# Performance work log

Measured on AMD Instinct MI355X. Metric: run time of the kernel, lower is better.

## Reference

```python
import jax, jax.numpy as jnp
import numpy as np

B, C, H, W = 32, 512, 32, 32
R = C // 2  # reduced channels for key/prod projections


def setup_inputs() -> dict:
    key = jax.random.key(0)
    ks = jax.random.split(key, 8)
    s_in = 1.0 / np.sqrt(C)
    return {
        "x": jax.random.normal(ks[0], (B, C, H, W), jnp.float32),
        "Wk": jax.random.normal(ks[1], (R, C), jnp.float32) * s_in,
        "bk": jax.random.normal(ks[2], (R,), jnp.float32) * s_in,
        "Wp": jax.random.normal(ks[3], (R, C), jnp.float32) * s_in,
        "bp": jax.random.normal(ks[4], (R,), jnp.float32) * s_in,
        "Wv": jax.random.normal(ks[5], (C, C), jnp.float32) * s_in,
        "bv": jax.random.normal(ks[6], (C,), jnp.float32) * s_in,
        "param": jax.random.normal(ks[7], (1,), jnp.float32),
    }


def _conv1x1(x, Wmat, b):
    # 1x1 conv on NCHW == per-pixel channel matmul
    return jnp.einsum('bchw,oc->bohw', x, Wmat) + b[None, :, None, None]


def reference(x, Wk, bk, Wp, bp, Wv, bv, param):
    b, c, h, w = x.shape
    hw = h * w
    f_key = _conv1x1(x, Wk, bk).reshape(b, -1, hw).transpose(0, 2, 1)  # [B,HW,R]
    f_prod = _conv1x1(x, Wp, bp).reshape(b, -1, hw)                    # [B,R,HW]
    f_value = _conv1x1(x, Wv, bv).reshape(b, -1, hw)                   # [B,C,HW]
    energy = jnp.einsum('bnr,brm->bnm', f_key, f_prod)                 # [B,HW,HW]
    similarity = jax.nn.softmax(energy, axis=-1)
    # bmm(f_value, similarity^T): out[b,c,n] = sum_m f_value[b,c,m] * sim[b,n,m]
    attended = jnp.einsum('bcm,bnm->bcn', f_value, similarity).reshape(b, c, h, w)
    return x + attended * param
```

## Files before the change

### kernel.cpp

```cpp
#include <hip/hip_runtime.h>
#include <hip/hip_bf16.h>

#define BATCH 32
#define CCH   512
#define HWSZ  1024
#define RCH   256

typedef __attribute__((ext_vector_type(8))) _Float16 f16x8;
typedef __attribute__((ext_vector_type(4))) float f32x4;

__device__ __forceinline__ ushort f2h(float f) {
    _Float16 h = (_Float16)f;
    ushort u; __builtin_memcpy(&u, &h, 2);
    return u;
}

__device__ __forceinline__ void load_lds16(const void* g, void* l) {
    __builtin_amdgcn_global_load_lds((const __attribute__((address_space(1))) void*)g,
                                     (__attribute__((address_space(3))) void*)l,
                                     16, 0, 0);
}

__device__ __forceinline__ void xcd_swizzle(int& bx, int& by, int& bz) {
    int gx = gridDim.x, gy = gridDim.y;
    int n   = gx * gy * gridDim.z;
    int lin = bx + gx * (by + gy * bz);
    int cpx = n >> 3;
    int s = (lin & 7) * cpx + (lin >> 3);
    bx = s % gx; s /= gx;
    by = s % gy;
    bz = s / gy;
}

__global__ __launch_bounds__(256) void k_prep_w(
    const float* __restrict__ Wk, const float* __restrict__ bk,
    const float* __restrict__ Wp, const float* __restrict__ bp,
    const float* __restrict__ Wv,
    ushort* __restrict__ Wkp_h, ushort* __restrict__ Wv_h, float* __restrict__ bias_kp)
{
    int idx = blockIdx.x * 256 + threadIdx.x;
    if (idx < 512 * 512) {
        int o = idx >> 9, c = idx & 511;
        float w = (o < 256) ? Wk[o * 512 + c] : Wp[(o - 256) * 512 + c];
        Wkp_h[idx] = f2h(w);
        Wv_h[idx]  = f2h(Wv[idx]);
        if (c == 0) bias_kp[o] = (o < 256) ? bk[o] : bp[o - 256];
    }
}

__global__ __launch_bounds__(256) void k_transpose(
    const float* __restrict__ x, ushort* __restrict__ xt)
{
    __shared__ float tile[64][65];
    int b  = blockIdx.z;
    int c0 = blockIdx.y * 64;
    int n0 = blockIdx.x * 64;
    const float* xb = x + (size_t)b * CCH * HWSZ;
    int t  = threadIdx.x;
    int tq = t >> 6;
    int tl = t & 63;
    #pragma unroll
    for (int i = 0; i < 16; ++i) {
        int c = i * 4 + tq;
        tile[c][tl] = xb[(size_t)(c0 + c) * HWSZ + n0 + tl];
    }
    __syncthreads();
    ushort* oh = xt + (size_t)b * HWSZ * CCH;
    #pragma unroll
    for (int i = 0; i < 16; ++i) {
        int n = i * 4 + tq;
        oh[(size_t)(n0 + n) * CCH + c0 + tl] = f2h(tile[tl][n]);
    }
}

template<int MODE>
__global__ __launch_bounds__(512, 2) void k_gemm8(
    const ushort* __restrict__ A, const ushort* __restrict__ B,
    int lda, int ldb, long aBatch, long bBatch,
    float* __restrict__ outF, ushort* __restrict__ out16,
    long oBatch, int ldo,
    const float* __restrict__ bias,
    const float* __restrict__ xres, const float* __restrict__ param,
    int NT)
{
    __shared__ ushort lds[2][2][2][8192];
    int bx = blockIdx.x, by = blockIdx.y, bz = blockIdx.z;
    xcd_swizzle(bx, by, bz);
    const int z  = bz;
    const int m0 = bx * 256;
    const int n0 = by * 256;
    const int t    = threadIdx.x;
    const int lane = t & 63;
    const int w    = t >> 6;
    const int wm = w >> 2, wn = w & 3;
    const int l15 = lane & 15;
    const int G   = (lane >> 4) ^ ((lane >> 1) & 3);

    const ushort* Ab = A + (size_t)z * aBatch;
    const ushort* Bb = B + (size_t)z * bBatch;

    const int sr = t >> 2;
    const int sg = (t & 3) ^ ((t >> 3) & 3);

    f32x4 acc[8][4] = {};
    f16x8 a[8], b[2];

#define STAGE(par, op, ks, kt) do {                                          \
        const ushort* gb_ = (op) ? Bb : Ab;                                  \
        int ld_ = (op) ? ldb : lda;                                          \
        int r0_ = (op) ? n0 : m0;                                            \
        size_t src_ = (size_t)(r0_ + sr) * ld_ + (kt) * 64 + (ks) * 32 + sg * 8; \
        load_lds16(gb_ + src_, &lds[par][op][ks][t * 8]);                    \
        load_lds16(gb_ + src_ + (size_t)128 * ld_, &lds[par][op][ks][t * 8 + 4096]); \
    } while (0)

#define LDA_(cur, ks) do {                                                   \
        _Pragma("unroll")                                                    \
        for (int mi = 0; mi < 8; ++mi)                                       \
            a[mi] = *(const f16x8*)&lds[cur][0][ks][(wm * 128 + mi * 16 + l15) * 32 + G * 8]; \
    } while (0)

#define LDB_(cur, ks, nh) do {                                               \
        _Pragma("unroll")                                                    \
        for (int ni = 0; ni < 2; ++ni)                                       \
            b[ni] = *(const f16x8*)&lds[cur][1][ks][(wn * 64 + (nh) * 32 + ni * 16 + l15) * 32 + G * 8]; \
    } while (0)

#define BAR() __builtin_amdgcn_s_barrier()

#define MFMA_BLK(nh) do {                                                    \
        asm volatile("s_waitcnt lgkmcnt(0)" ::: "memory");                   \
        __builtin_amdgcn_sched_barrier(0);                                   \
        __builtin_amdgcn_s_setprio(1);                                       \
        _Pragma("unroll")                                                    \
        for (int mi = 0; mi < 8; ++mi) {                                     \
            acc[mi][(nh)*2+0] = __builtin_amdgcn_mfma_f32_16x16x32_f16(a[mi], b[0], acc[mi][(nh)*2+0], 0, 0, 0); \
            acc[mi][(nh)*2+1] = __builtin_amdgcn_mfma_f32_16x16x32_f16(a[mi], b[1], acc[mi][(nh)*2+1], 0, 0, 0); \
        }                                                                    \
        __builtin_amdgcn_s_setprio(0);                                       \
    } while (0)

    STAGE(0, 0, 0, 0); STAGE(0, 1, 0, 0); STAGE(0, 0, 1, 0); STAGE(0, 1, 1, 0);
    asm volatile("s_waitcnt vmcnt(4)" ::: "memory");
    BAR();

    for (int j = 0; j < NT - 1; ++j) {
        int cur = j & 1, nxt = cur ^ 1;
        STAGE(nxt, 0, 0, j + 1);
        LDA_(cur, 0); LDB_(cur, 0, 0);
        BAR();
        MFMA_BLK(0);
        BAR();
        STAGE(nxt, 1, 0, j + 1);
        LDB_(cur, 0, 1);
        BAR();
        MFMA_BLK(1);
        asm volatile("s_waitcnt vmcnt(4)" ::: "memory");
        BAR();
        STAGE(nxt, 0, 1, j + 1);
        LDA_(cur, 1); LDB_(cur, 1, 0);
        BAR();
        MFMA_BLK(0);
        BAR();
        STAGE(nxt, 1, 1, j + 1);
        LDB_(cur, 1, 1);
        BAR();
        MFMA_BLK(1);
        asm volatile("s_waitcnt vmcnt(4)" ::: "memory");
        BAR();
    }
    {
        int cur = (NT - 1) & 1;
        LDA_(cur, 0); LDB_(cur, 0, 0);
        BAR();
        MFMA_BLK(0);
        BAR();
        LDB_(cur, 0, 1);
        BAR();
        MFMA_BLK(1);
        asm volatile("s_waitcnt vmcnt(0)" ::: "memory");
        BAR();
        LDA_(cur, 1); LDB_(cur, 1, 0);
        BAR();
        MFMA_BLK(0);
        BAR();
        LDB_(cur, 1, 1);
        BAR();
        MFMA_BLK(1);
    }

    const float prm = (MODE == 3) ? param[0] : 0.f;
    #pragma unroll
    for (int mi = 0; mi < 8; ++mi) {
        #pragma unroll
        for (int ni = 0; ni < 4; ++ni) {
            int gc  = n0 + wn * 64 + (ni >> 1) * 32 + (ni & 1) * 16 + l15;
            int gr0 = m0 + wm * 128 + mi * 16 + (lane >> 4) * 4;
            if (MODE == 3) {
                float*       ob = outF + (size_t)z * oBatch;
                const float* xb = xres + (size_t)z * oBatch;
                size_t g = (size_t)gc * ldo + gr0;
                float4 xv = *(const float4*)&xb[g];
                float4 ov;
                ov.x = xv.x + acc[mi][ni][0] * prm;
                ov.y = xv.y + acc[mi][ni][1] * prm;
                ov.z = xv.z + acc[mi][ni][2] * prm;
                ov.w = xv.w + acc[mi][ni][3] * prm;
                *(float4*)&ob[g] = ov;
            } else {
                #pragma unroll
                for (int jj = 0; jj < 4; ++jj) {
                    int gr = gr0 + jj;
                    float v = acc[mi][ni][jj];
                    if (MODE == 0) {
                        v += bias[gc];
                        out16[(size_t)gr * ldo + gc] = f2h(v);
                    } else if (MODE == 1) {
                        v += bias[gr];
                        out16[(size_t)z * oBatch + (size_t)gr * ldo + gc] = f2h(v);
                    } else {
                        outF[(size_t)z * oBatch + (size_t)gr * ldo + gc] = v;
                    }
                }
            }
        }
    }
#undef STAGE
#undef LDA_
#undef LDB_
#undef BAR
#undef MFMA_BLK
}

__global__ __launch_bounds__(256) void k_softmax(float* __restrict__ E)
{
    int blk = blockIdx.x;
    float* row = E + (size_t)blk * HWSZ;
    int t = threadIdx.x;
    float4 v = *(const float4*)&row[t * 4];
    float mx = fmaxf(fmaxf(v.x, v.y), fmaxf(v.z, v.w));
    #pragma unroll
    for (int off = 1; off < 64; off <<= 1)
        mx = fmaxf(mx, __shfl_xor(mx, off));
    __shared__ float redm[4];
    __shared__ float reds[4];
    int lane = t & 63, wv = t >> 6;
    if (lane == 0) redm[wv] = mx;
    __syncthreads();
    mx = fmaxf(fmaxf(redm[0], redm[1]), fmaxf(redm[2], redm[3]));
    float e0 = __expf(v.x - mx), e1 = __expf(v.y - mx);
    float e2 = __expf(v.z - mx), e3 = __expf(v.w - mx);
    float s = (e0 + e1) + (e2 + e3);
    #pragma unroll
    for (int off = 1; off < 64; off <<= 1)
        s += __shfl_xor(s, off);
    if (lane == 0) reds[wv] = s;
    __syncthreads();
    s = (reds[0] + reds[1]) + (reds[2] + reds[3]);
    float inv = 1.0f / s;
    ushort4 o;
    o.x = f2h(e0 * inv); o.y = f2h(e1 * inv);
    o.z = f2h(e2 * inv); o.w = f2h(e3 * inv);
    *(ushort4*)((ushort*)row + t * 4) = o;
}

extern "C" void kernel_launch(void* const* d_in, const int* in_sizes, int n_in,
                              void* d_out, int out_size, void* d_ws, size_t ws_size,
                              hipStream_t stream)
{
    const float* x    = (const float*)d_in[0];
    const float* Wk   = (const float*)d_in[1];
    const float* bk   = (const float*)d_in[2];
    const float* Wp   = (const float*)d_in[3];
    const float* bp   = (const float*)d_in[4];
    const float* Wv   = (const float*)d_in[5];
    const float* bv   = (const float*)d_in[6];
    const float* prm  = (const float*)d_in[7];
    float* out = (float*)d_out;
    char* ws = (char*)d_ws;

    const size_t SZ16 = (size_t)BATCH * HWSZ * CCH * 2;
    ushort* xt    = (ushort*)(ws + 0);
    ushort* KPt   = (ushort*)(ws + SZ16);
    ushort* fv    = (ushort*)(ws + 2 * SZ16);
    float*  E     = (float*)(ws + 3 * SZ16);
    char* wbase   = ws + 3 * SZ16 + (size_t)BATCH * HWSZ * HWSZ * 4;
    ushort* Wkp_h = (ushort*)(wbase);
    ushort* Wv_h  = (ushort*)(wbase + 524288);
    float*  bias_kp = (float*)(wbase + 2 * 524288);

    k_prep_w<<<1024, 256, 0, stream>>>(Wk, bk, Wp, bp, Wv, Wkp_h, Wv_h, bias_kp);
    k_transpose<<<dim3(16, 8, 32), 256, 0, stream>>>(x, xt);

    k_gemm8<0><<<dim3(128, 2, 1), 512, 0, stream>>>(
        xt, Wkp_h, CCH, CCH, 0, 0,
        nullptr, KPt, 0, CCH,
        bias_kp, nullptr, nullptr, CCH / 64);

    k_gemm8<1><<<dim3(2, 4, 32), 512, 0, stream>>>(
        Wv_h, xt, CCH, CCH, 0, (long)HWSZ * CCH,
        nullptr, fv, (long)CCH * HWSZ, HWSZ,
        bv, nullptr, nullptr, CCH / 64);

    k_gemm8<2><<<dim3(4, 4, 32), 512, 0, stream>>>(
        KPt, KPt + RCH, CCH, CCH,
        (long)HWSZ * CCH, (long)HWSZ * CCH,
        E, nullptr, (long)HWSZ * HWSZ, HWSZ,
        nullptr, nullptr, nullptr, RCH / 64);

    k_softmax<<<BATCH * HWSZ, 256, 0, stream>>>(E);

    k_gemm8<3><<<dim3(4, 2, 32), 512, 0, stream>>>(
        (const ushort*)E, fv, 2048, HWSZ,
        (long)HWSZ * 2048, (long)CCH * HWSZ,
        out, nullptr, (long)CCH * HWSZ, HWSZ,
        nullptr, x, prm, HWSZ / 64);
}
```

Measured before the change: 214.1 us.

## Double-buffer LDS fragments in registers and overlap reads with MFMA in GEMM loop

Rewrites the GEMM main loop so fragments for the next sub-step are read from LDS into a second set of registers while MFMAs run on the current set. Full lgkmcnt(0) waits become partial waits, and the loop now has two barriers per K-tile instead of eight. The loop is unrolled in pairs with a peeled final tile, which assumes an even tile count. The goal is to hide LDS latency and barrier stalls behind matrix math. In exchange it raises VGPR use and relies on the fewer barriers still being enough to avoid LDS races.

```diff
diff --git a/kernel.cpp b/kernel.cpp
--- a/kernel.cpp
+++ b/kernel.cpp
@@ -103,7 +103,7 @@
     const int sg = (t & 3) ^ ((t >> 3) & 3);
 
     f32x4 acc[8][4] = {};
-    f16x8 a[8], b[2];
+    f16x8 a0[8], a1[8], b01a[2], b23a[2], b01b[2], b23b[2];
 
 #define STAGE(par, op, ks, kt) do {                                          \
         const ushort* gb_ = (op) ? Bb : Ab;                                  \
@@ -114,79 +114,83 @@
         load_lds16(gb_ + src_ + (size_t)128 * ld_, &lds[par][op][ks][t * 8 + 4096]); \
     } while (0)
 
-#define LDA_(cur, ks) do {                                                   \
+#define RD_A(dst, par, ks) do {                                              \
         _Pragma("unroll")                                                    \
         for (int mi = 0; mi < 8; ++mi)                                       \
-            a[mi] = *(const f16x8*)&lds[cur][0][ks][(wm * 128 + mi * 16 + l15) * 32 + G * 8]; \
-    } while (0)
-
-#define LDB_(cur, ks, nh) do {                                               \
+            dst[mi] = *(const f16x8*)&lds[par][0][ks][(wm * 128 + mi * 16 + l15) * 32 + G * 8]; \
+    } while (0)
+
+#define RD_B(dst, par, ks, nh) do {                                          \
         _Pragma("unroll")                                                    \
         for (int ni = 0; ni < 2; ++ni)                                       \
-            b[ni] = *(const f16x8*)&lds[cur][1][ks][(wn * 64 + (nh) * 32 + ni * 16 + l15) * 32 + G * 8]; \
+            dst[ni] = *(const f16x8*)&lds[par][1][ks][(wn * 64 + (nh) * 32 + ni * 16 + l15) * 32 + G * 8]; \
     } while (0)
 
 #define BAR() __builtin_amdgcn_s_barrier()
-
-#define MFMA_BLK(nh) do {                                                    \
-        asm volatile("s_waitcnt lgkmcnt(0)" ::: "memory");                   \
-        __builtin_amdgcn_sched_barrier(0);                                   \
+#define WAIT_LGKM(N) do { asm volatile("s_waitcnt lgkmcnt(" #N ")" ::: "memory"); \
+                          __builtin_amdgcn_sched_barrier(0); } while (0)
+#define WAIT_VM(N)   do { asm volatile("s_waitcnt vmcnt(" #N ")" ::: "memory"); } while (0)
+
+#define MFMA16(av, bv, nh) do {                                              \
         __builtin_amdgcn_s_setprio(1);                                       \
         _Pragma("unroll")                                                    \
         for (int mi = 0; mi < 8; ++mi) {                                     \
-            acc[mi][(nh)*2+0] = __builtin_amdgcn_mfma_f32_16x16x32_f16(a[mi], b[0], acc[mi][(nh)*2+0], 0, 0, 0); \
-            acc[mi][(nh)*2+1] = __builtin_amdgcn_mfma_f32_16x16x32_f16(a[mi], b[1], acc[mi][(nh)*2+1], 0, 0, 0); \
+            acc[mi][(nh)*2+0] = __builtin_amdgcn_mfma_f32_16x16x32_f16(av[mi], bv[0], acc[mi][(nh)*2+0], 0, 0, 0); \
+            acc[mi][(nh)*2+1] = __builtin_amdgcn_mfma_f32_16x16x32_f16(av[mi], bv[1], acc[mi][(nh)*2+1], 0, 0, 0); \
         }                                                                    \
         __builtin_amdgcn_s_setprio(0);                                       \
     } while (0)
 
+#define TILE(cur, kt) do {                                                   \
+                                                                     \
+        STAGE(cur ^ 1, 0, 0, (kt) + 1);                                      \
+        RD_B(b23a, cur, 0, 1);                                               \
+        WAIT_LGKM(2);                                                        \
+        MFMA16(a0, b01a, 0);                                                 \
+                                                                     \
+        STAGE(cur ^ 1, 1, 0, (kt) + 1);                                      \
+        WAIT_VM(4); BAR();                                                   \
+        RD_A(a1, cur, 1); RD_B(b01b, cur, 1, 0);                             \
+        WAIT_LGKM(10);                                                       \
+        MFMA16(a0, b23a, 1);                                                 \
+                                                                     \
+        STAGE(cur ^ 1, 0, 1, (kt) + 1);                                      \
+        RD_B(b23b, cur, 1, 1);                                               \
+        WAIT_LGKM(2);                                                        \
+        MFMA16(a1, b01b, 0);                                                 \
+                                                                     \
+        STAGE(cur ^ 1, 1, 1, (kt) + 1);                                      \
+        WAIT_VM(4); BAR();                                                   \
+        RD_A(a0, cur ^ 1, 0); RD_B(b01a, cur ^ 1, 0, 0);                     \
+        WAIT_LGKM(10);                                                       \
+        MFMA16(a1, b23b, 1);                                                 \
+    } while (0)
+
     STAGE(0, 0, 0, 0); STAGE(0, 1, 0, 0); STAGE(0, 0, 1, 0); STAGE(0, 1, 1, 0);
-    asm volatile("s_waitcnt vmcnt(4)" ::: "memory");
+    WAIT_VM(4);
     BAR();
-
-    for (int j = 0; j < NT - 1; ++j) {
-        int cur = j & 1, nxt = cur ^ 1;
-        STAGE(nxt, 0, 0, j + 1);
-        LDA_(cur, 0); LDB_(cur, 0, 0);
-        BAR();
-        MFMA_BLK(0);
-        BAR();
-        STAGE(nxt, 1, 0, j + 1);
-        LDB_(cur, 0, 1);
-        BAR();
-        MFMA_BLK(1);
-        asm volatile("s_waitcnt vmcnt(4)" ::: "memory");
-        BAR();
-        STAGE(nxt, 0, 1, j + 1);
-        LDA_(cur, 1); LDB_(cur, 1, 0);
-        BAR();
-        MFMA_BLK(0);
-        BAR();
-        STAGE(nxt, 1, 1, j + 1);
-        LDB_(cur, 1, 1);
-        BAR();
-        MFMA_BLK(1);
-        asm volatile("s_waitcnt vmcnt(4)" ::: "memory");
-        BAR();
-    }
+    RD_A(a0, 0, 0); RD_B(b01a, 0, 0, 0);
+
+    const int nPair = (NT - 1) >> 1;
+    for (int jj = 0; jj < nPair; ++jj) {
+        TILE(0, 2 * jj);
+        TILE(1, 2 * jj + 1);
+    }
+    TILE(0, NT - 2);
+
     {
-        int cur = (NT - 1) & 1;
-        LDA_(cur, 0); LDB_(cur, 0, 0);
-        BAR();
-        MFMA_BLK(0);
-        BAR();
-        LDB_(cur, 0, 1);
-        BAR();
-        MFMA_BLK(1);
-        asm volatile("s_waitcnt vmcnt(0)" ::: "memory");
-        BAR();
-        LDA_(cur, 1); LDB_(cur, 1, 0);
-        BAR();
-        MFMA_BLK(0);
-        BAR();
-        LDB_(cur, 1, 1);
-        BAR();
-        MFMA_BLK(1);
+        RD_B(b23a, 1, 0, 1);
+        WAIT_LGKM(2);
+        MFMA16(a0, b01a, 0);
+        WAIT_VM(0); BAR();
+        RD_A(a1, 1, 1); RD_B(b01b, 1, 1, 0);
+        WAIT_LGKM(10);
+        MFMA16(a0, b23a, 1);
+        RD_B(b23b, 1, 1, 1);
+        WAIT_LGKM(2);
+        MFMA16(a1, b01b, 0);
+        WAIT_LGKM(0);
+        MFMA16(a1, b23b, 1);
     }
 
     const float prm = (MODE == 3) ? param[0] : 0.f;
@@ -226,10 +230,13 @@
         }
     }
 #undef STAGE
-#undef LDA_
-#undef LDB_
+#undef RD_A
+#undef RD_B
 #undef BAR
-#undef MFMA_BLK
+#undef WAIT_LGKM
+#undef WAIT_VM
+#undef MFMA16
+#undef TILE
 }
 
 __global__ __launch_bounds__(256) void k_softmax(float* __restrict__ E)
```

New measurement: 225.8 us. +5.4%, slower.
